# Kernel tuning notes

Measured on AMD Instinct MI355X. Metric: run time of the kernel, lower is better.

Reference implementation:

```python
import jax, jax.numpy as jnp
import numpy as np

NP, NR, NK = 64, 8, 500          # problems, rollouts, candidate nodes
H, HEADS, VD = 256, 8, 8         # hidden_dim, heads, vars_dim
HD = H // HEADS                  # head_dim
CLIP = 10.0                      # tanh logit clipping
NEG_INF = -jnp.inf


def setup_inputs() -> dict:
    key = jax.random.key(0)
    ks = jax.random.split(key, 17)
    f = lambda k, s: jax.random.normal(k, s, dtype=jnp.float32)
    B = NP * NR
    s = 1.0 / np.sqrt(H)
    return {
        "X": f(ks[0], (NP, NK, H)),
        "K": f(ks[1], (HEADS, NP, NK, HD)),
        "V": f(ks[2], (HEADS, NP, NK, HD)),
        "query": f(ks[3], (B, H)),
        "state1": f(ks[4], (B, H)),
        "state2": f(ks[5], (B, H)),
        "varfeat": f(ks[6], (NP, VD, NK)),
        "mask": jax.random.uniform(ks[7], (NP, NR, NK)) < 0.1,
        "nn_Q": f(ks[8], (HEADS, H, HD)) * (1.0 / np.sqrt(HD)),
        "nn_O": f(ks[9], (H, H)) * s,
        "nn_A": f(ks[10], (VD, H)) * s,
        "nn_B": f(ks[11], (H,)) * s,
        "nn_W": f(ks[12], (H,)) * s,
        "W_ih": f(ks[13], (4 * H, H)) * s,
        "W_hh": f(ks[14], (4 * H, H)) * s,
        "b_ih": f(ks[15], (4 * H,)) * s,
        "b_hh": f(ks[16], (4 * H,)) * s,
    }


def _decode(X, K, V, query, state1, state2, varfeat, mask,
            nn_Q, nn_O, nn_A, nn_B, nn_W, W_ih, W_hh, b_ih, b_hh):
    B = query.shape[0]
    # --- LSTMCell (PyTorch gate order: i, f, g, o) ---
    gates = query @ W_ih.T + b_ih + state1 @ W_hh.T + b_hh
    i, fg, g, o = jnp.split(gates, 4, axis=1)
    c = jax.nn.sigmoid(fg) * state2 + jax.nn.sigmoid(i) * jnp.tanh(g)
    h = jax.nn.sigmoid(o) * jnp.tanh(c)
    # --- MultiHeadAttention (glimpse) ---
    q = h.reshape(NP, NR, H)
    Q = jnp.einsum('pqh,ahd->apqd', q, nn_Q)                    # [heads,NP,NR,HD]
    S = jnp.einsum('apqd,apkd->apqk', Q, K) * (1.0 / np.sqrt(HD))
    S = jnp.where(mask[None], NEG_INF, S)
    S = jax.nn.softmax(S, axis=-1)
    x = jnp.einsum('apqk,apkd->apqd', S, V)
    x = x.transpose(1, 2, 0, 3).reshape(NP, NR, H)              # [NP,NR,H]
    qm = x @ nn_O                                               # glimpse query
    # --- additive attention with variable features ---
    vf = jnp.einsum('pvk,vh->pkh', varfeat, nn_A) + nn_B        # [NP,NK,H]
    t = jnp.tanh(X[:, None] + vf[:, None] + qm[:, :, None])     # [NP,NR,NK,H]
    logit = jnp.einsum('pqkh,h->pqk', t, nn_W)
    logit = jnp.where(mask, NEG_INF, logit).reshape(B, NK)
    # --- choose (mode=1: greedy argmax) ---
    infeasible = logit == NEG_INF
    l = jnp.where(infeasible, NEG_INF, jnp.tanh(logit) * CLIP)
    chosen = jnp.argmax(l, axis=1)
    logp = jax.nn.log_softmax(l, axis=1)
    chosen_p = jnp.take_along_axis(logp, chosen[:, None], axis=1).squeeze(1)
    return h, c, chosen_p


def reference(X, K, V, query, state1, state2, varfeat, mask,
              nn_Q, nn_O, nn_A, nn_B, nn_W, W_ih, W_hh, b_ih, b_hh):
    return _decode(X, K, V, query, state1, state2, varfeat, mask,
                   nn_Q, nn_O, nn_A, nn_B, nn_W, W_ih, W_hh, b_ih, b_hh)
```

## Files before the change

### kernel.cpp

```cpp
#include <hip/hip_runtime.h>

#define NPP   64
#define NRR   8
#define NKK   500
#define HDIM  256
#define NHEAD 8
#define VDIM  8
#define HD    32
#define BTOT  512

__device__ __forceinline__ float fast_tanh(float x) {
  const float e = __expf(2.f * x);
  return 1.f - 2.f * __builtin_amdgcn_rcpf(e + 1.f);
}
__device__ __forceinline__ float fast_sig(float x) {
  return __builtin_amdgcn_rcpf(1.f + __expf(-x));
}
__device__ __forceinline__ float sigf(float x) { return 1.f / (1.f + expf(-x)); }

__global__ __launch_bounds__(256) void k_lstm3(
    const float* __restrict__ query, const float* __restrict__ state1,
    const float* __restrict__ state2,
    const float* __restrict__ W_ih, const float* __restrict__ W_hh,
    const float* __restrict__ b_ih, const float* __restrict__ b_hh,
    float* __restrict__ out_h, float* __restrict__ out_c)
{
  __shared__ float Wt[32][33];
  __shared__ float At[32][33];
  __shared__ float gt[32][33];

  const int t  = threadIdx.x;
  const int hb = blockIdx.x;
  const int bb = blockIdx.y;

  const int trow = t >> 4;
  const int tcol = t & 15;

  float acc00 = 0.f, acc01 = 0.f, acc10 = 0.f, acc11 = 0.f;

  const int wrow = t >> 3, wk4 = t & 7;
  const int wpart = wrow >> 3, whh = wrow & 7;
  const int wgrow = wpart * HDIM + hb * 8 + whh;
  const int agrow = bb * 32 + wrow;

  for (int k0 = 0; k0 < 512; k0 += 32) {
    __syncthreads();
    {
      const float* wsrc = (k0 < 256) ? (W_ih + (size_t)wgrow * HDIM + k0)
                                     : (W_hh + (size_t)wgrow * HDIM + (k0 - 256));
      const float4 wv = *reinterpret_cast<const float4*>(wsrc + wk4 * 4);
      Wt[wk4 * 4 + 0][wrow] = wv.x; Wt[wk4 * 4 + 1][wrow] = wv.y;
      Wt[wk4 * 4 + 2][wrow] = wv.z; Wt[wk4 * 4 + 3][wrow] = wv.w;

      const float* asrc = (k0 < 256) ? (query  + (size_t)agrow * HDIM + k0)
                                     : (state1 + (size_t)agrow * HDIM + (k0 - 256));
      const float4 av = *reinterpret_cast<const float4*>(asrc + wk4 * 4);
      At[wk4 * 4 + 0][wrow] = av.x; At[wk4 * 4 + 1][wrow] = av.y;
      At[wk4 * 4 + 2][wrow] = av.z; At[wk4 * 4 + 3][wrow] = av.w;
    }
    __syncthreads();

#pragma unroll 8
    for (int kk = 0; kk < 32; ++kk) {
      const float w0 = Wt[kk][trow], w1 = Wt[kk][trow + 16];
      const float a0 = At[kk][tcol], a1 = At[kk][tcol + 16];
      acc00 += w0 * a0; acc01 += w0 * a1;
      acc10 += w1 * a0; acc11 += w1 * a1;
    }
  }

  gt[trow][tcol] = acc00;      gt[trow][tcol + 16] = acc01;
  gt[trow + 16][tcol] = acc10; gt[trow + 16][tcol + 16] = acc11;
  __syncthreads();

  {
    const int h = t & 7, b = t >> 3;
    const int gh = hb * 8 + h;
    const int gb = bb * 32 + b;
    const float bi = b_ih[0 * HDIM + gh] + b_hh[0 * HDIM + gh];
    const float bf = b_ih[1 * HDIM + gh] + b_hh[1 * HDIM + gh];
    const float bg = b_ih[2 * HDIM + gh] + b_hh[2 * HDIM + gh];
    const float bo = b_ih[3 * HDIM + gh] + b_hh[3 * HDIM + gh];
    const float iv = fast_sig (gt[ 0 + h][b] + bi);
    const float fv = fast_sig (gt[ 8 + h][b] + bf);
    const float gv = fast_tanh(gt[16 + h][b] + bg);
    const float ov = fast_sig (gt[24 + h][b] + bo);
    const size_t off = (size_t)gb * HDIM + gh;
    const float c = fv * state2[off] + iv * gv;
    out_c[off] = c;
    out_h[off] = ov * fast_tanh(c);
  }
}

__global__ __launch_bounds__(1024) void k_attn5(
    const float* __restrict__ Kt, const float* __restrict__ Vt,
    const float* __restrict__ nn_Q, const float* __restrict__ nn_O,
    const void* __restrict__ maskp,
    const float* __restrict__ out_h, float* __restrict__ qm)
{
  const int p = blockIdx.x >> 3;
  const int a = blockIdx.x & 7;
  const int t = threadIdx.x;
  const int wave = t >> 6, lane = t & 63;

  __shared__ float hs[NRR][HDIM];
  __shared__ float buf[HDIM * 33];
  __shared__ float Qs[NRR][HD];
  __shared__ float Sb[NRR][NKK];
  __shared__ float xs[NRR][HD];
  __shared__ int   mask_any;

  const unsigned char* mb = (const unsigned char*)maskp;
  const int* mi = (const int*)maskp;

  if (t == 0) mask_any = 0;
  __syncthreads();
  {
    int any = 0;
    for (int j = t; j < 2048; j += 1024) any |= mb[2 * j + 1];
    if (any) atomicOr(&mask_any, 1);
  }

  if (t < 512)
    reinterpret_cast<float4*>(&hs[0][0])[t] =
        reinterpret_cast<const float4*>(out_h + (size_t)p * NRR * HDIM)[t];
  {
    const float4* nq4 = reinterpret_cast<const float4*>(
        nn_Q + (size_t)a * HDIM * HD);
    for (int idx = t; idx < 2048; idx += 1024) {
      const int h = idx >> 3, d4 = idx & 7;
      const float4 v = nq4[idx];
      buf[h * 33 + d4 * 4 + 0] = v.x;
      buf[h * 33 + d4 * 4 + 1] = v.y;
      buf[h * 33 + d4 * 4 + 2] = v.z;
      buf[h * 33 + d4 * 4 + 3] = v.w;
    }
  }
  __syncthreads();
  const bool mbyte = (mask_any != 0);

  {
    const int r = t >> 7, d = (t >> 2) & 31, c = t & 3;
    float acc = 0.f;
#pragma unroll 8
    for (int h = c * 64; h < c * 64 + 64; ++h)
      acc += hs[r][h] * buf[h * 33 + d];
    float* qp = &Sb[0][0];
    qp[((r * HD) + d) * 4 + c] = acc;
  }
  __syncthreads();
  if (t < 256) {
    const int r = t >> 5, d = t & 31;
    const float* qp = &Sb[0][0];
    Qs[r][d] = (qp[(r * HD + d) * 4 + 0] + qp[(r * HD + d) * 4 + 1]
              + qp[(r * HD + d) * 4 + 2] + qp[(r * HD + d) * 4 + 3])
             * 0.17677669529663687f;
  }
  __syncthreads();

  {
    const int k2 = t >> 1;
    const int dh = t & 1;
    const int kc = (k2 < NKK) ? k2 : (NKK - 1);
    const float4* kr4 = reinterpret_cast<const float4*>(
        Kt + (((size_t)a * NPP + p) * NKK + kc) * HD + dh * 16);
    float sc[NRR];
#pragma unroll
    for (int r = 0; r < NRR; ++r) sc[r] = 0.f;
#pragma unroll
    for (int c4 = 0; c4 < 4; ++c4) {
      const float4 u = kr4[c4];
#pragma unroll
      for (int r = 0; r < NRR; ++r) {
        sc[r] += Qs[r][dh * 16 + c4 * 4 + 0] * u.x
               + Qs[r][dh * 16 + c4 * 4 + 1] * u.y
               + Qs[r][dh * 16 + c4 * 4 + 2] * u.z
               + Qs[r][dh * 16 + c4 * 4 + 3] * u.w;
      }
    }
#pragma unroll
    for (int r = 0; r < NRR; ++r) sc[r] += __shfl_xor(sc[r], 1, 64);
    if (dh == 0 && k2 < NKK) {
#pragma unroll
      for (int r = 0; r < NRR; ++r) {
        const size_t mrow = (size_t)(p * NRR + r) * NKK + k2;
        const bool mk = mbyte ? (mb[mrow] != 0) : (mi[mrow] != 0);
        Sb[r][k2] = mk ? -INFINITY : sc[r];
      }
    }
  }
  __syncthreads();

  if (wave < NRR) {
    const int r = wave;
    float m = -INFINITY;
    for (int k = lane; k < NKK; k += 64) m = fmaxf(m, Sb[r][k]);
#pragma unroll
    for (int off = 32; off > 0; off >>= 1) m = fmaxf(m, __shfl_xor(m, off, 64));
    float ssum = 0.f;
    for (int k = lane; k < NKK; k += 64) {
      const float e = __expf(Sb[r][k] - m);
      Sb[r][k] = e;
      ssum += e;
    }
#pragma unroll
    for (int off = 32; off > 0; off >>= 1) ssum += __shfl_xor(ssum, off, 64);
    const float inv = 1.f / ssum;
    for (int k = lane; k < NKK; k += 64) Sb[r][k] *= inv;
  }
  __syncthreads();

  {
    const int d = t & 31, ks = t >> 5;
    float acc[NRR];
#pragma unroll
    for (int r = 0; r < NRR; ++r) acc[r] = 0.f;
    const float* vb = Vt + ((size_t)a * NPP + p) * NKK * HD + d;
    for (int k = ks; k < NKK; k += 32) {
      const float v = vb[(size_t)k * HD];
#pragma unroll
      for (int r = 0; r < NRR; ++r) acc[r] += Sb[r][k] * v;
    }
#pragma unroll
    for (int r = 0; r < NRR; ++r) buf[(ks * NRR + r) * HD + d] = acc[r];
  }
  __syncthreads();
  if (t < 256) {
    const int r = t >> 5, d = t & 31;
    float s = 0.f;
#pragma unroll
    for (int ks = 0; ks < 32; ++ks) s += buf[(ks * NRR + r) * HD + d];
    xs[r][d] = s;
  }
  __syncthreads();

  {
    const int j = t & 255, rr = t >> 8;
    const int r0 = rr * 2;
    float a0 = 0.f, a1 = 0.f;
#pragma unroll 8
    for (int d = 0; d < HD; ++d) {
      const float w = nn_O[((size_t)(a * HD + d)) * HDIM + j];
      a0 += xs[r0][d] * w;
      a1 += xs[r0 + 1][d] * w;
    }
    atomicAdd(&qm[(size_t)(p * NRR + r0) * HDIM + j], a0);
    atomicAdd(&qm[(size_t)(p * NRR + r0 + 1) * HDIM + j], a1);
  }
}

__global__ __launch_bounds__(256) void k_logits3(
    const float* __restrict__ X, const float* __restrict__ varfeat,
    const float* __restrict__ nn_A, const float* __restrict__ nn_B,
    const float* __restrict__ nn_W, const float* __restrict__ qm,
    const void* __restrict__ maskp, float* __restrict__ ls)
{
  const int p  = blockIdx.x >> 5;
  const int kt = blockIdx.x & 31;
  const int t = threadIdx.x;
  const int wave = t >> 6, lane = t & 63;
  const int h0 = lane * 4;

  __shared__ float As[VDIM][260];
  __shared__ float Ws[HDIM];
  __shared__ float qb[NRR][260];
  __shared__ int   mask_any;

  const unsigned char* mb = (const unsigned char*)maskp;
  const int* mi = (const int*)maskp;

  if (t == 0) mask_any = 0;
  __syncthreads();
  {
    int any = 0;
    for (int j = t; j < 2048; j += 256) any |= mb[2 * j + 1];
    if (any) atomicOr(&mask_any, 1);
  }

  for (int idx = t; idx < VDIM * HDIM; idx += 256)
    As[idx >> 8][idx & 255] = nn_A[idx];
  Ws[t] = nn_W[t];
  for (int idx = t; idx < NRR * HDIM; idx += 256) {
    const int r = idx >> 8, h = idx & 255;
    qb[r][h] = qm[(size_t)(p * NRR + r) * HDIM + h] + nn_B[h];
  }
  __syncthreads();
  const bool mbyte = (mask_any != 0);

  const float4 w4 = *reinterpret_cast<const float4*>(&Ws[h0]);

  for (int kk = 0; kk < 4; ++kk) {
    const int k = kt * 16 + wave * 4 + kk;
    if (k >= NKK) break;

    const float4 x4 = *reinterpret_cast<const float4*>(
        X + ((size_t)p * NKK + k) * HDIM + h0);
    float base0 = x4.x, base1 = x4.y, base2 = x4.z, base3 = x4.w;
#pragma unroll
    for (int v = 0; v < VDIM; ++v) {
      const float vv = varfeat[((size_t)p * VDIM + v) * NKK + k];
      const float4 a4 = *reinterpret_cast<const float4*>(&As[v][h0]);
      base0 += vv * a4.x; base1 += vv * a4.y;
      base2 += vv * a4.z; base3 += vv * a4.w;
    }

    float acc[NRR];
#pragma unroll
    for (int r = 0; r < NRR; ++r) {
      const float4 q4 = *reinterpret_cast<const float4*>(&qb[r][h0]);
      acc[r] = fast_tanh(base0 + q4.x) * w4.x + fast_tanh(base1 + q4.y) * w4.y
             + fast_tanh(base2 + q4.z) * w4.z + fast_tanh(base3 + q4.w) * w4.w;
    }

    float v4[4];
    {
      float sw[8];
#pragma unroll
      for (int j = 0; j < 8; ++j) sw[j] = __shfl_xor(acc[j], 32, 64);
      const bool hi = (lane & 32) != 0;
#pragma unroll
      for (int j = 0; j < 4; ++j)
        v4[j] = hi ? (acc[j + 4] + sw[j + 4]) : (acc[j] + sw[j]);
    }
    float v2[2];
    {
      float sw[4];
#pragma unroll
      for (int j = 0; j < 4; ++j) sw[j] = __shfl_xor(v4[j], 16, 64);
      const bool hi = (lane & 16) != 0;
      v2[0] = hi ? (v4[2] + sw[2]) : (v4[0] + sw[0]);
      v2[1] = hi ? (v4[3] + sw[3]) : (v4[1] + sw[1]);
    }
    float w;
    {
      const float s0 = __shfl_xor(v2[0], 8, 64);
      const float s1 = __shfl_xor(v2[1], 8, 64);
      w = ((lane & 8) != 0) ? (v2[1] + s1) : (v2[0] + s0);
    }
    w += __shfl_xor(w, 4, 64);
    w += __shfl_xor(w, 2, 64);
    w += __shfl_xor(w, 1, 64);

    if ((lane & 7) == 0) {
      const int r = lane >> 3;
      const size_t mrow = (size_t)(p * NRR + r) * NKK + k;
      const bool mk = mbyte ? (mb[mrow] != 0) : (mi[mrow] != 0);
      ls[mrow] = mk ? -INFINITY : fast_tanh(w) * 10.0f;
    }
  }
}

__global__ __launch_bounds__(64) void k_choose(
    const float* __restrict__ ls, float* __restrict__ out_p)
{
  const int b = blockIdx.x;
  const int lane = threadIdx.x;
  float m = -INFINITY;
  float lv[8];
  int n = 0;
  for (int k = lane; k < NKK; k += 64, ++n) {
    lv[n] = ls[(size_t)b * NKK + k];
    m = fmaxf(m, lv[n]);
  }
#pragma unroll
  for (int off = 32; off > 0; off >>= 1) m = fmaxf(m, __shfl_xor(m, off, 64));
  float s = 0.f;
  for (int i = 0; i < n; ++i) s += __expf(lv[i] - m);
#pragma unroll
  for (int off = 32; off > 0; off >>= 1) s += __shfl_xor(s, off, 64);
  if (lane == 0) out_p[b] = -logf(s);
}

__global__ __launch_bounds__(256) void k_fused(
    const float* __restrict__ X, const float* __restrict__ Kt,
    const float* __restrict__ Vt, const float* __restrict__ varfeat,
    const void* __restrict__ maskp,
    const float* __restrict__ nn_Q, const float* __restrict__ nn_O,
    const float* __restrict__ nn_A, const float* __restrict__ nn_B,
    const float* __restrict__ nn_W,
    const float* __restrict__ out_h, float* __restrict__ out_p)
{
  const int p = blockIdx.x >> 3;
  const int r = blockIdx.x & 7;
  const int t = threadIdx.x;
  const int wave = t >> 6, lane = t & 63;

  __shared__ float hs[HDIM];
  __shared__ float Qs[NHEAD][HD];
  __shared__ float Sb[NHEAD][NKK];
  __shared__ float xs[HDIM];
  __shared__ float qs[HDIM];
  __shared__ float As2[HDIM][VDIM];
  __shared__ float Ws[HDIM];
  __shared__ float lsb[NKK];
  __shared__ int   mask_any;

  const unsigned char* mb = (const unsigned char*)maskp;
  if (t == 0) mask_any = 0;
  __syncthreads();
  {
    int any = 0;
    for (int j = t; j < 2048; j += 256) any |= mb[2 * j + 1];
    if (any) atomicOr(&mask_any, 1);
  }
  for (int idx = t; idx < VDIM * HDIM; idx += 256)
    As2[idx & 255][idx >> 8] = nn_A[idx];
  Ws[t] = nn_W[t];
  hs[t] = out_h[(size_t)(p * NRR + r) * HDIM + t];
  __syncthreads();
  const bool mbyte = (mask_any != 0);
  const int* mi = (const int*)maskp;
  const size_t mrow = (size_t)(p * NRR + r) * NKK;
  {
    const int a = t >> 5, d = t & 31;
    const float* nq = nn_Q + (size_t)a * HDIM * HD + d;
    float acc = 0.f;
    for (int h = 0; h < HDIM; ++h) acc += hs[h] * nq[(size_t)h * HD];
    Qs[a][d] = acc * 0.17677669529663687f;
  }
  __syncthreads();
  for (int k = t; k < NKK; k += 256) {
    const bool mk = mbyte ? (mb[mrow + k] != 0) : (mi[mrow + k] != 0);
#pragma unroll
    for (int a = 0; a < NHEAD; ++a) {
      const float4* kr4 = reinterpret_cast<const float4*>(
          Kt + (((size_t)a * NPP + p) * NKK + k) * HD);
      float s = 0.f;
#pragma unroll
      for (int d4 = 0; d4 < HD / 4; ++d4) {
        const float4 u = kr4[d4];
        s += Qs[a][4 * d4] * u.x + Qs[a][4 * d4 + 1] * u.y
           + Qs[a][4 * d4 + 2] * u.z + Qs[a][4 * d4 + 3] * u.w;
      }
      Sb[a][k] = mk ? -INFINITY : s;
    }
  }
  __syncthreads();
  for (int aa = 0; aa < 2; ++aa) {
    const int a = wave * 2 + aa;
    float m = -INFINITY;
    for (int k = lane; k < NKK; k += 64) m = fmaxf(m, Sb[a][k]);
#pragma unroll
    for (int off = 32; off > 0; off >>= 1) m = fmaxf(m, __shfl_xor(m, off, 64));
    float ssum = 0.f;
    for (int k = lane; k < NKK; k += 64) {
      const float e = expf(Sb[a][k] - m);
      Sb[a][k] = e; ssum += e;
    }
#pragma unroll
    for (int off = 32; off > 0; off >>= 1) ssum += __shfl_xor(ssum, off, 64);
    const float inv = 1.f / ssum;
    for (int k = lane; k < NKK; k += 64) Sb[a][k] *= inv;
  }
  __syncthreads();
  {
    const int a = t >> 5, d = t & 31;
    const float* vb = Vt + ((size_t)a * NPP + p) * NKK * HD + d;
    float acc = 0.f;
    for (int k = 0; k < NKK; ++k) acc += Sb[a][k] * vb[(size_t)k * HD];
    xs[a * HD + d] = acc;
  }
  __syncthreads();
  {
    float acc = 0.f;
    for (int i = 0; i < HDIM; ++i) acc += xs[i] * nn_O[(size_t)i * HDIM + t];
    qs[t] = acc + nn_B[t];
  }
  __syncthreads();
  for (int k = t; k < NKK; k += 256) {
    float vfv[VDIM];
#pragma unroll
    for (int v = 0; v < VDIM; ++v)
      vfv[v] = varfeat[((size_t)p * VDIM + v) * NKK + k];
    const float4* xp4 = reinterpret_cast<const float4*>(
        X + ((size_t)p * NKK + k) * HDIM);
    float acc = 0.f;
    for (int h4 = 0; h4 < HDIM / 4; ++h4) {
      const float4 ux = xp4[h4];
      const float xv[4] = {ux.x, ux.y, ux.z, ux.w};
#pragma unroll
      for (int j = 0; j < 4; ++j) {
        const int h = 4 * h4 + j;
        float base = xv[j] + qs[h];
        const float4 a0 = *reinterpret_cast<const float4*>(&As2[h][0]);
        const float4 a1 = *reinterpret_cast<const float4*>(&As2[h][4]);
        base += vfv[0] * a0.x + vfv[1] * a0.y + vfv[2] * a0.z + vfv[3] * a0.w
              + vfv[4] * a1.x + vfv[5] * a1.y + vfv[6] * a1.z + vfv[7] * a1.w;
        acc += tanhf(base) * Ws[h];
      }
    }
    lsb[k] = acc;
  }
  __syncthreads();
  for (int k = t; k < NKK; k += 256) {
    const bool mk = mbyte ? (mb[mrow + k] != 0) : (mi[mrow + k] != 0);
    lsb[k] = mk ? -INFINITY : tanhf(lsb[k]) * 10.0f;
  }
  __syncthreads();
  if (wave == 0) {
    float m = -INFINITY;
    for (int k = lane; k < NKK; k += 64) m = fmaxf(m, lsb[k]);
#pragma unroll
    for (int off = 32; off > 0; off >>= 1) m = fmaxf(m, __shfl_xor(m, off, 64));
    float s = 0.f;
    for (int k = lane; k < NKK; k += 64) s += expf(lsb[k] - m);
#pragma unroll
    for (int off = 32; off > 0; off >>= 1) s += __shfl_xor(s, off, 64);
    if (lane == 0) out_p[p * NRR + r] = -logf(s);
  }
}

extern "C" void kernel_launch(void* const* d_in, const int* in_sizes, int n_in,
                              void* d_out, int out_size, void* d_ws, size_t ws_size,
                              hipStream_t stream)
{
  const float* X       = (const float*)d_in[0];
  const float* Kt      = (const float*)d_in[1];
  const float* Vt      = (const float*)d_in[2];
  const float* query   = (const float*)d_in[3];
  const float* state1  = (const float*)d_in[4];
  const float* state2  = (const float*)d_in[5];
  const float* varfeat = (const float*)d_in[6];
  const void*  maskp   = d_in[7];
  const float* nn_Q    = (const float*)d_in[8];
  const float* nn_O    = (const float*)d_in[9];
  const float* nn_A    = (const float*)d_in[10];
  const float* nn_B    = (const float*)d_in[11];
  const float* nn_W    = (const float*)d_in[12];
  const float* W_ih    = (const float*)d_in[13];
  const float* W_hh    = (const float*)d_in[14];
  const float* b_ih    = (const float*)d_in[15];
  const float* b_hh    = (const float*)d_in[16];

  float* out   = (float*)d_out;
  float* out_h = out;
  float* out_c = out + (size_t)BTOT * HDIM;
  float* out_p = out + (size_t)2 * BTOT * HDIM;

  hipLaunchKernelGGL(k_lstm3, dim3(32, 16), dim3(256), 0, stream,
                     query, state1, state2, W_ih, W_hh, b_ih, b_hh,
                     out_h, out_c);

  const size_t qm_bytes = (size_t)BTOT * HDIM * 4;
  const size_t ls_bytes = (size_t)BTOT * NKK * 4;
  if (ws_size >= qm_bytes + ls_bytes) {
    float* qmw = (float*)d_ws;
    float* lsw = (float*)((char*)d_ws + qm_bytes);
    hipMemsetAsync(qmw, 0, qm_bytes, stream);
    hipLaunchKernelGGL(k_attn5, dim3(NPP * NHEAD), dim3(1024), 0, stream,
                       Kt, Vt, nn_Q, nn_O, maskp, out_h, qmw);
    hipLaunchKernelGGL(k_logits3, dim3(NPP * 32), dim3(256), 0, stream,
                       X, varfeat, nn_A, nn_B, nn_W, qmw, maskp, lsw);
    hipLaunchKernelGGL(k_choose, dim3(BTOT), dim3(64), 0, stream,
                       lsw, out_p);
  } else {
    hipLaunchKernelGGL(k_fused, dim3(NPP * NRR), dim3(256), 0, stream,
                       X, Kt, Vt, varfeat, maskp,
                       nn_Q, nn_O, nn_A, nn_B, nn_W,
                       out_h, out_p);
  }
}
```

Baseline: 235.4 us.

## Prefetch K/V into registers, hoist mask check, replace qm atomics with slabs

Computes the mask-dtype flag once in the LSTM kernel and passes it to later kernels instead of re-scanning the mask in every block. The attention kernel now issues its K, V, nn_Q and mask loads up front into registers so their latency overlaps the Q projection. When the workspace is large enough, per-head partial qm results go to separate slabs, which removes the memset and atomics; the logits kernel then sums 8 slabs. This costs extra registers, which may lower occupancy, plus 8x workspace traffic for qm.

```diff
diff --git a/kernel.cpp b/kernel.cpp
--- a/kernel.cpp
+++ b/kernel.cpp
@@ -16,13 +16,13 @@
 __device__ __forceinline__ float fast_sig(float x) {
   return __builtin_amdgcn_rcpf(1.f + __expf(-x));
 }
-__device__ __forceinline__ float sigf(float x) { return 1.f / (1.f + expf(-x)); }
 
 __global__ __launch_bounds__(256) void k_lstm3(
     const float* __restrict__ query, const float* __restrict__ state1,
     const float* __restrict__ state2,
     const float* __restrict__ W_ih, const float* __restrict__ W_hh,
     const float* __restrict__ b_ih, const float* __restrict__ b_hh,
+    const unsigned char* __restrict__ maskb, int* __restrict__ flagp,
     float* __restrict__ out_h, float* __restrict__ out_c)
 {
   __shared__ float Wt[32][33];
@@ -32,6 +32,17 @@
   const int t  = threadIdx.x;
   const int hb = blockIdx.x;
   const int bb = blockIdx.y;
+
+  if (flagp != nullptr && hb == 0 && bb == 0) {
+    __shared__ int f;
+    if (t == 0) f = 0;
+    __syncthreads();
+    int any = 0;
+    for (int j = t; j < 2048; j += 256) any |= maskb[2 * j + 1];
+    if (any) atomicOr(&f, 1);
+    __syncthreads();
+    if (t == 0) *flagp = f;
+  }
 
   const int trow = t >> 4;
   const int tcol = t & 15;
@@ -92,11 +103,11 @@
   }
 }
 
-__global__ __launch_bounds__(1024) void k_attn5(
+__global__ __launch_bounds__(1024) void k_attn6(
     const float* __restrict__ Kt, const float* __restrict__ Vt,
     const float* __restrict__ nn_Q, const float* __restrict__ nn_O,
-    const void* __restrict__ maskp,
-    const float* __restrict__ out_h, float* __restrict__ qm)
+    const void* __restrict__ maskp, const int* __restrict__ flagp,
+    const float* __restrict__ out_h, float* __restrict__ qmw, int use_slabs)
 {
   const int p = blockIdx.x >> 3;
   const int a = blockIdx.x & 7;
@@ -108,36 +119,56 @@
   __shared__ float Qs[NRR][HD];
   __shared__ float Sb[NRR][NKK];
   __shared__ float xs[NRR][HD];
-  __shared__ int   mask_any;
 
   const unsigned char* mb = (const unsigned char*)maskp;
   const int* mi = (const int*)maskp;
 
-  if (t == 0) mask_any = 0;
-  __syncthreads();
-  {
-    int any = 0;
-    for (int j = t; j < 2048; j += 1024) any |= mb[2 * j + 1];
-    if (any) atomicOr(&mask_any, 1);
-  }
-
+  float4 hv = make_float4(0.f, 0.f, 0.f, 0.f);
   if (t < 512)
-    reinterpret_cast<float4*>(&hs[0][0])[t] =
-        reinterpret_cast<const float4*>(out_h + (size_t)p * NRR * HDIM)[t];
-  {
-    const float4* nq4 = reinterpret_cast<const float4*>(
-        nn_Q + (size_t)a * HDIM * HD);
-    for (int idx = t; idx < 2048; idx += 1024) {
-      const int h = idx >> 3, d4 = idx & 7;
-      const float4 v = nq4[idx];
-      buf[h * 33 + d4 * 4 + 0] = v.x;
-      buf[h * 33 + d4 * 4 + 1] = v.y;
-      buf[h * 33 + d4 * 4 + 2] = v.z;
-      buf[h * 33 + d4 * 4 + 3] = v.w;
-    }
-  }
-  __syncthreads();
-  const bool mbyte = (mask_any != 0);
+    hv = reinterpret_cast<const float4*>(out_h + (size_t)p * NRR * HDIM)[t];
+  const float4* nq4 = reinterpret_cast<const float4*>(nn_Q + (size_t)a * HDIM * HD);
+  const float4 q0 = nq4[t];
+  const float4 q1 = nq4[t + 1024];
+
+  const int flag = *flagp;
+
+  const int k2 = t >> 1, dh = t & 1;
+  const int kc = (k2 < NKK) ? k2 : (NKK - 1);
+  const float4 kreg = *reinterpret_cast<const float4*>(
+      Kt + (((size_t)a * NPP + p) * NKK + kc) * HD + dh * 16);
+
+  const int dpv = t & 31, kspv = t >> 5;
+  const float* vb = Vt + ((size_t)a * NPP + p) * NKK * HD + dpv;
+  float vreg[16];
+#pragma unroll
+  for (int j = 0; j < 15; ++j) vreg[j] = vb[(size_t)(kspv + 32 * j) * HD];
+  vreg[15] = (kspv < NKK - 480) ? vb[(size_t)(kspv + 480) * HD] : 0.f;
+
+  float maskval[NRR];
+#pragma unroll
+  for (int r = 0; r < NRR; ++r) maskval[r] = 0.f;
+  if (dh == 0 && k2 < NKK) {
+    if (flag) {
+#pragma unroll
+      for (int r = 0; r < NRR; ++r)
+        maskval[r] = mb[(size_t)(p * NRR + r) * NKK + k2] ? -INFINITY : 0.f;
+    } else {
+#pragma unroll
+      for (int r = 0; r < NRR; ++r)
+        maskval[r] = mi[(size_t)(p * NRR + r) * NKK + k2] ? -INFINITY : 0.f;
+    }
+  }
+
+  if (t < 512) reinterpret_cast<float4*>(&hs[0][0])[t] = hv;
+  {
+    const int h0 = t >> 3, d40 = t & 7;
+    buf[h0 * 33 + d40 * 4 + 0] = q0.x; buf[h0 * 33 + d40 * 4 + 1] = q0.y;
+    buf[h0 * 33 + d40 * 4 + 2] = q0.z; buf[h0 * 33 + d40 * 4 + 3] = q0.w;
+    const int h1 = (t + 1024) >> 3, d41 = t & 7;
+    buf[h1 * 33 + d41 * 4 + 0] = q1.x; buf[h1 * 33 + d41 * 4 + 1] = q1.y;
+    buf[h1 * 33 + d41 * 4 + 2] = q1.z; buf[h1 * 33 + d41 * 4 + 3] = q1.w;
+  }
+  __syncthreads();
 
   {
     const int r = t >> 7, d = (t >> 2) & 31, c = t & 3;
@@ -159,34 +190,40 @@
   __syncthreads();
 
   {
-    const int k2 = t >> 1;
-    const int dh = t & 1;
-    const int kc = (k2 < NKK) ? k2 : (NKK - 1);
+    float sc[NRR];
+#pragma unroll
+    for (int r = 0; r < NRR; ++r) sc[r] = 0.f;
+#pragma unroll
+    for (int c4 = 0; c4 < 4; ++c4) {
+      const float u[4] = {c4 == 0 ? kreg.x : (c4 == 1 ? kreg.x : kreg.x)};
+      (void)u;
+    }
+    {
+      const float4 u = kreg;
+#pragma unroll
+      for (int r = 0; r < NRR; ++r) {
+        sc[r] += Qs[r][dh * 16 + 0] * u.x + Qs[r][dh * 16 + 1] * u.y
+               + Qs[r][dh * 16 + 2] * u.z + Qs[r][dh * 16 + 3] * u.w;
+      }
+    }
     const float4* kr4 = reinterpret_cast<const float4*>(
         Kt + (((size_t)a * NPP + p) * NKK + kc) * HD + dh * 16);
-    float sc[NRR];
-#pragma unroll
-    for (int r = 0; r < NRR; ++r) sc[r] = 0.f;
-#pragma unroll
-    for (int c4 = 0; c4 < 4; ++c4) {
-      const float4 u = kr4[c4];
-#pragma unroll
-      for (int r = 0; r < NRR; ++r) {
-        sc[r] += Qs[r][dh * 16 + c4 * 4 + 0] * u.x
-               + Qs[r][dh * 16 + c4 * 4 + 1] * u.y
-               + Qs[r][dh * 16 + c4 * 4 + 2] * u.z
-               + Qs[r][dh * 16 + c4 * 4 + 3] * u.w;
-      }
+    const float4 u1 = kr4[1], u2 = kr4[2], u3 = kr4[3];
+#pragma unroll
+    for (int r = 0; r < NRR; ++r) {
+      sc[r] += Qs[r][dh * 16 +  4] * u1.x + Qs[r][dh * 16 +  5] * u1.y
+             + Qs[r][dh * 16 +  6] * u1.z + Qs[r][dh * 16 +  7] * u1.w
+             + Qs[r][dh * 16 +  8] * u2.x + Qs[r][dh * 16 +  9] * u2.y
+             + Qs[r][dh * 16 + 10] * u2.z + Qs[r][dh * 16 + 11] * u2.w
+             + Qs[r][dh * 16 + 12] * u3.x + Qs[r][dh * 16 + 13] * u3.y
+             + Qs[r][dh * 16 + 14] * u3.z + Qs[r][dh * 16 + 15] * u3.w;
     }
 #pragma unroll
     for (int r = 0; r < NRR; ++r) sc[r] += __shfl_xor(sc[r], 1, 64);
     if (dh == 0 && k2 < NKK) {
 #pragma unroll
-      for (int r = 0; r < NRR; ++r) {
-        const size_t mrow = (size_t)(p * NRR + r) * NKK + k2;
-        const bool mk = mbyte ? (mb[mrow] != 0) : (mi[mrow] != 0);
-        Sb[r][k2] = mk ? -INFINITY : sc[r];
-      }
+      for (int r = 0; r < NRR; ++r)
+        Sb[r][k2] = sc[r] + maskval[r];
     }
   }
   __syncthreads();
@@ -211,18 +248,24 @@
   __syncthreads();
 
   {
-    const int d = t & 31, ks = t >> 5;
     float acc[NRR];
 #pragma unroll
     for (int r = 0; r < NRR; ++r) acc[r] = 0.f;
-    const float* vb = Vt + ((size_t)a * NPP + p) * NKK * HD + d;
-    for (int k = ks; k < NKK; k += 32) {
-      const float v = vb[(size_t)k * HD];
+#pragma unroll
+    for (int j = 0; j < 15; ++j) {
+      const int k = kspv + 32 * j;
+      const float v = vreg[j];
 #pragma unroll
       for (int r = 0; r < NRR; ++r) acc[r] += Sb[r][k] * v;
     }
-#pragma unroll
-    for (int r = 0; r < NRR; ++r) buf[(ks * NRR + r) * HD + d] = acc[r];
+    if (kspv < NKK - 480) {
+      const int k = kspv + 480;
+      const float v = vreg[15];
+#pragma unroll
+      for (int r = 0; r < NRR; ++r) acc[r] += Sb[r][k] * v;
+    }
+#pragma unroll
+    for (int r = 0; r < NRR; ++r) buf[(kspv * NRR + r) * HD + dpv] = acc[r];
   }
   __syncthreads();
   if (t < 256) {
@@ -244,15 +287,22 @@
       a0 += xs[r0][d] * w;
       a1 += xs[r0 + 1][d] * w;
     }
-    atomicAdd(&qm[(size_t)(p * NRR + r0) * HDIM + j], a0);
-    atomicAdd(&qm[(size_t)(p * NRR + r0 + 1) * HDIM + j], a1);
-  }
-}
-
-__global__ __launch_bounds__(256) void k_logits3(
+    if (use_slabs) {
+      float* slab = qmw + (size_t)a * BTOT * HDIM;
+      slab[(size_t)(p * NRR + r0) * HDIM + j] = a0;
+      slab[(size_t)(p * NRR + r0 + 1) * HDIM + j] = a1;
+    } else {
+      atomicAdd(&qmw[(size_t)(p * NRR + r0) * HDIM + j], a0);
+      atomicAdd(&qmw[(size_t)(p * NRR + r0 + 1) * HDIM + j], a1);
+    }
+  }
+}
+
+__global__ __launch_bounds__(256) void k_logits4(
     const float* __restrict__ X, const float* __restrict__ varfeat,
     const float* __restrict__ nn_A, const float* __restrict__ nn_B,
-    const float* __restrict__ nn_W, const float* __restrict__ qm,
+    const float* __restrict__ nn_W, const float* __restrict__ qmw,
+    int use_slabs, const int* __restrict__ flagp,
     const void* __restrict__ maskp, float* __restrict__ ls)
 {
   const int p  = blockIdx.x >> 5;
@@ -264,28 +314,30 @@
   __shared__ float As[VDIM][260];
   __shared__ float Ws[HDIM];
   __shared__ float qb[NRR][260];
-  __shared__ int   mask_any;
 
   const unsigned char* mb = (const unsigned char*)maskp;
   const int* mi = (const int*)maskp;
 
-  if (t == 0) mask_any = 0;
-  __syncthreads();
-  {
-    int any = 0;
-    for (int j = t; j < 2048; j += 256) any |= mb[2 * j + 1];
-    if (any) atomicOr(&mask_any, 1);
-  }
+  const int flag = *flagp;
 
   for (int idx = t; idx < VDIM * HDIM; idx += 256)
     As[idx >> 8][idx & 255] = nn_A[idx];
   Ws[t] = nn_W[t];
   for (int idx = t; idx < NRR * HDIM; idx += 256) {
     const int r = idx >> 8, h = idx & 255;
-    qb[r][h] = qm[(size_t)(p * NRR + r) * HDIM + h] + nn_B[h];
-  }
-  __syncthreads();
-  const bool mbyte = (mask_any != 0);
+    float q;
+    if (use_slabs) {
+      q = 0.f;
+#pragma unroll
+      for (int a = 0; a < NHEAD; ++a)
+        q += qmw[(size_t)a * BTOT * HDIM + (size_t)(p * NRR + r) * HDIM + h];
+    } else {
+      q = qmw[(size_t)(p * NRR + r) * HDIM + h];
+    }
+    qb[r][h] = q + nn_B[h];
+  }
+  __syncthreads();
+  const bool mbyte = (flag != 0);
 
   const float4 w4 = *reinterpret_cast<const float4*>(&Ws[h0]);
 
@@ -537,20 +589,30 @@
   float* out_c = out + (size_t)BTOT * HDIM;
   float* out_p = out + (size_t)2 * BTOT * HDIM;
 
+  const size_t flag_bytes = 256;
+  const size_t qm1_bytes  = (size_t)BTOT * HDIM * 4;
+  const size_t qm8_bytes  = (size_t)NHEAD * BTOT * HDIM * 4;
+  const size_t ls_bytes   = (size_t)BTOT * NKK * 4;
+
+  const bool slabs  = ws_size >= flag_bytes + qm8_bytes + ls_bytes;
+  const bool atomic = !slabs && ws_size >= flag_bytes + qm1_bytes + ls_bytes;
+  int* flagp = (slabs || atomic) ? (int*)d_ws : nullptr;
+
   hipLaunchKernelGGL(k_lstm3, dim3(32, 16), dim3(256), 0, stream,
                      query, state1, state2, W_ih, W_hh, b_ih, b_hh,
-                     out_h, out_c);
-
-  const size_t qm_bytes = (size_t)BTOT * HDIM * 4;
-  const size_t ls_bytes = (size_t)BTOT * NKK * 4;
-  if (ws_size >= qm_bytes + ls_bytes) {
-    float* qmw = (float*)d_ws;
-    float* lsw = (float*)((char*)d_ws + qm_bytes);
-    hipMemsetAsync(qmw, 0, qm_bytes, stream);
-    hipLaunchKernelGGL(k_attn5, dim3(NPP * NHEAD), dim3(1024), 0, stream,
-                       Kt, Vt, nn_Q, nn_O, maskp, out_h, qmw);
-    hipLaunchKernelGGL(k_logits3, dim3(NPP * 32), dim3(256), 0, stream,
-                       X, varfeat, nn_A, nn_B, nn_W, qmw, maskp, lsw);
+                     (const unsigned char*)maskp, flagp, out_h, out_c);
+
+  if (slabs || atomic) {
+    float* qmw = (float*)((char*)d_ws + flag_bytes);
+    float* lsw = (float*)((char*)d_ws + flag_bytes +
+                          (slabs ? qm8_bytes : qm1_bytes));
+    const int use_slabs = slabs ? 1 : 0;
+    if (!slabs) hipMemsetAsync(qmw, 0, qm1_bytes, stream);
+    hipLaunchKernelGGL(k_attn6, dim3(NPP * NHEAD), dim3(1024), 0, stream,
+                       Kt, Vt, nn_Q, nn_O, maskp, flagp, out_h, qmw, use_slabs);
+    hipLaunchKernelGGL(k_logits4, dim3(NPP * 32), dim3(256), 0, stream,
+                       X, varfeat, nn_A, nn_B, nn_W, qmw, use_slabs, flagp,
+                       maskp, lsw);
     hipLaunchKernelGGL(k_choose, dim3(BTOT), dim3(64), 0, stream,
                        lsw, out_p);
   } else {
```

Result: faster. 223.4 us (-5.1%).
